# Performance work log

Hardware: AMD Instinct MI355X
Metric: run time of the kernel (lower is better)

## Reference

```python
import jax, jax.numpy as jnp
import numpy as np

A0 = 0.5291772105638411
KE = 14.399645351950548
KEHALF = KE / 2.0


def _softplus_inverse(x):
    return float(np.log(np.expm1(x)))


def setup_inputs() -> dict:
    key = jax.random.key(0)
    k_nb, k_mask, k_z, k_r = jax.random.split(key, 4)
    B, A, K = 16, 1024, 1023
    neighbors = jax.random.randint(k_nb, (B, A, K), 0, A)
    neighbor_mask = (jax.random.uniform(k_mask, (B, A, K)) > 0.1).astype(jnp.float32)
    atomic_numbers = jax.random.randint(k_z, (B, A), 1, 95)
    r_ij = jax.random.uniform(k_r, (B, A, K), minval=0.5, maxval=10.0, dtype=jnp.float32)
    p = jnp.float32
    params = {
        "_adiv": jnp.full((1,), _softplus_inverse(1.0 / (0.8854 * A0)), p),
        "_apow": jnp.full((1,), _softplus_inverse(0.23), p),
        "_c1": jnp.full((1,), _softplus_inverse(0.1818), p),
        "_c2": jnp.full((1,), _softplus_inverse(0.5099), p),
        "_c3": jnp.full((1,), _softplus_inverse(0.2802), p),
        "_c4": jnp.full((1,), _softplus_inverse(0.02817), p),
        "_a1": jnp.full((1,), _softplus_inverse(3.2), p),
        "_a2": jnp.full((1,), _softplus_inverse(0.9423), p),
        "_a3": jnp.full((1,), _softplus_inverse(0.4028), p),
        "_a4": jnp.full((1,), _softplus_inverse(0.2016), p),
    }
    return dict(neighbors=neighbors, neighbor_mask=neighbor_mask,
                atomic_numbers=atomic_numbers, r_ij=r_ij, **params)


def reference(neighbors, neighbor_mask, atomic_numbers, r_ij,
              _adiv, _apow, _c1, _c2, _c3, _c4, _a1, _a2, _a3, _a4):
    sp = jax.nn.softplus
    B = neighbors.shape[0]
    Zf = atomic_numbers.astype(jnp.float32)            # [B, A]
    Zp = Zf ** sp(_apow)                               # [B, A] (param [1] broadcasts)
    bidx = jnp.arange(B)[:, None, None]                # batch index for gather
    # gather of symmetric pair quantities without materializing [B, A, A]:
    # a[b,i,j] = Zp[b,i] + Zp[b,j];  zizj[b,i,j] = Zf[b,i] * Zf[b,j]
    Zp_j = Zp[bidx, neighbors]                         # [B, A, K]
    Zf_j = Zf[bidx, neighbors]                         # [B, A, K]
    a = (Zp[:, :, None] + Zp_j) * sp(_adiv) * neighbor_mask
    zizj = Zf[:, :, None] * Zf_j * neighbor_mask
    # normalized mixture coefficients
    c1, c2, c3, c4 = sp(_c1), sp(_c2), sp(_c3), sp(_c4)
    csum = c1 + c2 + c3 + c4
    c1, c2, c3, c4 = c1 / csum, c2 / csum, c3 / csum, c4 / csum
    ar = a * r_ij
    f = (c1 * jnp.exp(-sp(_a1) * ar) + c2 * jnp.exp(-sp(_a2) * ar)
         + c3 * jnp.exp(-sp(_a3) * ar) + c4 * jnp.exp(-sp(_a4) * ar))
    valid = neighbor_mask != 0
    r_safe = jnp.where(valid, r_ij, 1.0)
    corr_ij = jnp.where(valid, KEHALF * f * zizj / r_safe, 0.0)
    return jnp.sum(corr_ij, axis=-1, keepdims=True)    # [B, A, 1]
```

## Files before the change

### kernel.cpp

```cpp
#include <hip/hip_runtime.h>
#include <math.h>

#define KEHALF_F 7.199822675975274f
#define A_ATOMS 1024
#define LOG2E_F 1.4426950408889634f
#define LN2_F   0.6931471805599453f

#if !__has_builtin(__builtin_amdgcn_exp2f)
extern "C" __device__ float __ocml_native_exp2_f32(float);
#endif
#if !__has_builtin(__builtin_amdgcn_logf)
extern "C" __device__ float __ocml_native_log2_f32(float);
#endif

__device__ __forceinline__ float fast_exp2(float x) {
#if __has_builtin(__builtin_amdgcn_exp2f)
    return __builtin_amdgcn_exp2f(x);
#else
    return __ocml_native_exp2_f32(x);
#endif
}
__device__ __forceinline__ float fast_log2(float x) {
#if __has_builtin(__builtin_amdgcn_logf)
    return __builtin_amdgcn_logf(x);
#else
    return __ocml_native_log2_f32(x);
#endif
}
__device__ __forceinline__ float softplus_f(float x) {
    return LN2_F * fast_log2(1.0f + fast_exp2(x * LOG2E_F));
}

__global__ __launch_bounds__(256) void zbl_pre_kernel(
    const int* __restrict__ atomic_numbers,
    const float* __restrict__ p_adiv, const float* __restrict__ p_apow,
    float2* __restrict__ tab, int n)
{
    const int i = blockIdx.x * 256 + threadIdx.x;
    if (i < n) {
        const float sp_apow = softplus_f(p_apow[0]);
        const float sp_adiv = softplus_f(p_adiv[0]);
        float zf = (float)atomic_numbers[i];
        tab[i] = make_float2(zf, fast_exp2(sp_apow * fast_log2(zf)) * sp_adiv);
    }
}

__global__ __launch_bounds__(512, 8) void zbl_main_kernel(
    const int* __restrict__ neighbors,
    const float* __restrict__ neighbor_mask,
    const float* __restrict__ r_ij,
    const float2* __restrict__ tab,
    const float* __restrict__ p_c1, const float* __restrict__ p_c2,
    const float* __restrict__ p_c3, const float* __restrict__ p_c4,
    const float* __restrict__ p_a1, const float* __restrict__ p_a2,
    const float* __restrict__ p_a3, const float* __restrict__ p_a4,
    float* __restrict__ out, int K)
{
    __shared__ float2 zz[A_ATOMS];

    const int tid = threadIdx.x;
    const int block_row_base = blockIdx.x << 4;
    const int b = block_row_base >> 10;

    ((float4*)zz)[tid] = ((const float4*)(tab + ((size_t)b << 10)))[tid];
    __syncthreads();

    float c1 = softplus_f(p_c1[0]), c2 = softplus_f(p_c2[0]);
    float c3 = softplus_f(p_c3[0]), c4 = softplus_f(p_c4[0]);
    const float inv_cs = 1.0f / (c1 + c2 + c3 + c4);
    c1 *= inv_cs; c2 *= inv_cs; c3 *= inv_cs; c4 *= inv_cs;
    const float b1 = -softplus_f(p_a1[0]) * LOG2E_F;
    const float b2 = -softplus_f(p_a2[0]) * LOG2E_F;
    const float b3 = -softplus_f(p_a3[0]) * LOG2E_F;
    const float b4 = -softplus_f(p_a4[0]) * LOG2E_F;

    const int wid  = tid >> 6;
    const int lane = tid & 63;

#define ZBL_TERM(J, M, R)                                                   \
    {                                                                       \
        float2 zj = zz[(J)];                                                \
        float ar = (ziy + zj.y) * (M) * (R);                                \
        float fe = c1 * fast_exp2(b1 * ar) + c2 * fast_exp2(b2 * ar)        \
                 + c3 * fast_exp2(b3 * ar) + c4 * fast_exp2(b4 * ar);       \
        acc += fe * __fdividef(zix * zj.x * (M), (R));                      \
    }

    #pragma unroll 1
    for (int p = 0; p < 2; ++p) {
        const int row = block_row_base + wid + (p << 3);

        const float2 zi = zz[row & (A_ATOMS - 1)];
        const float zix = KEHALF_F * zi.x;
        const float ziy = zi.y;

        const size_t base = (size_t)row * K;
        const int f = (int)((4 - (int)(base & 3)) & 3);
        const int ngroups = (K - f) >> 2;
        const int tailc   = (K - f) & 3;

        const int*   nb = neighbors     + base;
        const float* mk = neighbor_mask + base;
        const float* rr = r_ij          + base;
        const int4*   nb4 = (const int4*)  (nb + f);
        const float4* mk4 = (const float4*)(mk + f);
        const float4* rr4 = (const float4*)(rr + f);

        float acc = 0.0f;

        const int g0 = lane, g1 = lane + 64, g2 = lane + 128, g3 = lane + 192;
        const int g3c  = g3 < ngroups ? g3 : (ngroups - 1);
        const float w3 = g3 < ngroups ? 1.0f : 0.0f;

        int4   j0 = nb4[g0], j1 = nb4[g1], j2 = nb4[g2], j3 = nb4[g3c];
        float4 m0 = mk4[g0], m1 = mk4[g1], m2 = mk4[g2], m3 = mk4[g3c];
        float4 r0 = rr4[g0], r1 = rr4[g1], r2 = rr4[g2], r3 = rr4[g3c];
        m3.x *= w3; m3.y *= w3; m3.z *= w3; m3.w *= w3;

        ZBL_TERM(j0.x, m0.x, r0.x); ZBL_TERM(j0.y, m0.y, r0.y);
        ZBL_TERM(j0.z, m0.z, r0.z); ZBL_TERM(j0.w, m0.w, r0.w);
        ZBL_TERM(j1.x, m1.x, r1.x); ZBL_TERM(j1.y, m1.y, r1.y);
        ZBL_TERM(j1.z, m1.z, r1.z); ZBL_TERM(j1.w, m1.w, r1.w);
        ZBL_TERM(j2.x, m2.x, r2.x); ZBL_TERM(j2.y, m2.y, r2.y);
        ZBL_TERM(j2.z, m2.z, r2.z); ZBL_TERM(j2.w, m2.w, r2.w);
        ZBL_TERM(j3.x, m3.x, r3.x); ZBL_TERM(j3.y, m3.y, r3.y);
        ZBL_TERM(j3.z, m3.z, r3.z); ZBL_TERM(j3.w, m3.w, r3.w);

        int e = -1;
        if (lane < f)              e = lane;
        else if (lane - f < tailc) e = f + (ngroups << 2) + (lane - f);
        if (e >= 0) {
            int   j = nb[e];
            float m = mk[e];
            float r = rr[e];
            ZBL_TERM(j, m, r);
        }

        #pragma unroll
        for (int off = 32; off > 0; off >>= 1)
            acc += __shfl_down(acc, off, 64);
        if (lane == 0)
            out[row] = acc;
    }
#undef ZBL_TERM
}

extern "C" void kernel_launch(void* const* d_in, const int* in_sizes, int n_in,
                              void* d_out, int out_size, void* d_ws, size_t ws_size,
                              hipStream_t stream) {
    const int*   neighbors      = (const int*)  d_in[0];
    const float* neighbor_mask  = (const float*)d_in[1];
    const int*   atomic_numbers = (const int*)  d_in[2];
    const float* r_ij           = (const float*)d_in[3];

    float*  out = (float*)d_out;
    float2* tab = (float2*)d_ws;

    const int n = in_sizes[2];
    const int K = in_sizes[0] / n;

    zbl_pre_kernel<<<(n + 255) / 256, 256, 0, stream>>>(
        atomic_numbers, (const float*)d_in[4], (const float*)d_in[5], tab, n);

    zbl_main_kernel<<<n / 16, 512, 0, stream>>>(
        neighbors, neighbor_mask, r_ij, tab,
        (const float*)d_in[6], (const float*)d_in[7],
        (const float*)d_in[8], (const float*)d_in[9],
        (const float*)d_in[10], (const float*)d_in[11],
        (const float*)d_in[12], (const float*)d_in[13],
        out, K);
}
```

Baseline: 254.3 us.

## Software-pipeline row loads with double-buffered registers and 4 rows per wave

Each wave now handles four rows with 256-thread blocks, prefetching the next row's neighbor, mask and distance vectors into a second register set while the current row computes. The scalar tail is loaded unconditionally with a clamped index, the division becomes a hardware reciprocal, and four independent accumulators break the add dependency chain. The mask multiply is dropped from the exponent argument, and the table load is issued before the parameter softplus setup. The goal is to hide global-memory latency within a wave, at the cost of higher register pressure and fewer waves per block. Approximate reciprocal precision is also slightly lower.

```diff
diff --git a/kernel.cpp b/kernel.cpp
--- a/kernel.cpp
+++ b/kernel.cpp
@@ -25,6 +25,13 @@
     return __builtin_amdgcn_logf(x);
 #else
     return __ocml_native_log2_f32(x);
+#endif
+}
+__device__ __forceinline__ float fast_rcp(float x) {
+#if __has_builtin(__builtin_amdgcn_rcpf)
+    return __builtin_amdgcn_rcpf(x);
+#else
+    return __frcp_rn(x);
 #endif
 }
 __device__ __forceinline__ float softplus_f(float x) {
@@ -45,7 +52,95 @@
     }
 }
 
-__global__ __launch_bounds__(512, 8) void zbl_main_kernel(
+struct RowData {
+    int4   j0, j1, j2, j3;
+    float4 m0, m1, m2, m3;
+    float4 r0, r1, r2, r3;
+    float  w3;
+    int    js; float ms, rs;
+    int    row;
+};
+
+__device__ __forceinline__ void load_row(
+    RowData& d, int row,
+    const int* __restrict__ nbg, const float* __restrict__ mkg,
+    const float* __restrict__ rrg, int K, int lane)
+{
+    d.row = row;
+    const size_t base = (size_t)row * K;
+    const int f = (int)((4 - (int)(base & 3)) & 3);
+    const int ngroups = (K - f) >> 2;
+    const int tailc   = (K - f) & 3;
+
+    const int*   nb = nbg + base;
+    const float* mk = mkg + base;
+    const float* rr = rrg + base;
+    const int4*   nb4 = (const int4*)  (nb + f);
+    const float4* mk4 = (const float4*)(mk + f);
+    const float4* rr4 = (const float4*)(rr + f);
+
+    const int g0 = lane, g1 = lane + 64, g2 = lane + 128, g3 = lane + 192;
+    const int g3c = g3 < ngroups ? g3 : (ngroups - 1);
+    d.w3 = g3 < ngroups ? 1.0f : 0.0f;
+
+    d.j0 = nb4[g0]; d.j1 = nb4[g1]; d.j2 = nb4[g2]; d.j3 = nb4[g3c];
+    d.m0 = mk4[g0]; d.m1 = mk4[g1]; d.m2 = mk4[g2]; d.m3 = mk4[g3c];
+    d.r0 = rr4[g0]; d.r1 = rr4[g1]; d.r2 = rr4[g2]; d.r3 = rr4[g3c];
+
+    int e = -1;
+    if (lane < f)              e = lane;
+    else if (lane - f < tailc) e = f + (ngroups << 2) + (lane - f);
+    const int ec = e < 0 ? 0 : e;
+    d.js = nb[ec];
+    d.rs = rr[ec];
+    float msv = mk[ec];
+    d.ms = e >= 0 ? msv : 0.0f;
+}
+
+__device__ __forceinline__ void compute_row(
+    const RowData& d, const float2* zz,
+    float c1, float c2, float c3, float c4,
+    float b1, float b2, float b3, float b4,
+    float* __restrict__ out, int lane)
+{
+    const float2 zi = zz[d.row & (A_ATOMS - 1)];
+    const float zix = KEHALF_F * zi.x;
+    const float ziy = zi.y;
+
+    float acc0 = 0.0f, acc1 = 0.0f, acc2 = 0.0f, acc3 = 0.0f;
+
+#define ZBL_TERM(ACC, J, M, R)                                              \
+    {                                                                       \
+        float2 zj = zz[(J)];                                                \
+        float ar = (ziy + zj.y) * (R);            \
+        float fe = c1 * fast_exp2(b1 * ar) + c2 * fast_exp2(b2 * ar)        \
+                 + c3 * fast_exp2(b3 * ar) + c4 * fast_exp2(b4 * ar);       \
+        ACC += fe * (zix * zj.x * (M)) * fast_rcp(R);                       \
+    }
+
+    float4 m3 = d.m3;
+    m3.x *= d.w3; m3.y *= d.w3; m3.z *= d.w3; m3.w *= d.w3;
+
+    ZBL_TERM(acc0, d.j0.x, d.m0.x, d.r0.x); ZBL_TERM(acc1, d.j0.y, d.m0.y, d.r0.y);
+    ZBL_TERM(acc2, d.j0.z, d.m0.z, d.r0.z); ZBL_TERM(acc3, d.j0.w, d.m0.w, d.r0.w);
+    ZBL_TERM(acc0, d.j1.x, d.m1.x, d.r1.x); ZBL_TERM(acc1, d.j1.y, d.m1.y, d.r1.y);
+    ZBL_TERM(acc2, d.j1.z, d.m1.z, d.r1.z); ZBL_TERM(acc3, d.j1.w, d.m1.w, d.r1.w);
+    ZBL_TERM(acc0, d.j2.x, d.m2.x, d.r2.x); ZBL_TERM(acc1, d.j2.y, d.m2.y, d.r2.y);
+    ZBL_TERM(acc2, d.j2.z, d.m2.z, d.r2.z); ZBL_TERM(acc3, d.j2.w, d.m2.w, d.r2.w);
+    ZBL_TERM(acc0, d.j3.x, m3.x,   d.r3.x); ZBL_TERM(acc1, d.j3.y, m3.y,   d.r3.y);
+    ZBL_TERM(acc2, d.j3.z, m3.z,   d.r3.z); ZBL_TERM(acc3, d.j3.w, m3.w,   d.r3.w);
+    ZBL_TERM(acc0, d.js,   d.ms,   d.rs);
+#undef ZBL_TERM
+
+    float acc = (acc0 + acc1) + (acc2 + acc3);
+    #pragma unroll
+    for (int off = 32; off > 0; off >>= 1)
+        acc += __shfl_down(acc, off, 64);
+    if (lane == 0)
+        out[d.row] = acc;
+}
+
+__global__ __launch_bounds__(256) void zbl_main_kernel(
     const int* __restrict__ neighbors,
     const float* __restrict__ neighbor_mask,
     const float* __restrict__ r_ij,
@@ -62,8 +157,9 @@
     const int block_row_base = blockIdx.x << 4;
     const int b = block_row_base >> 10;
 
-    ((float4*)zz)[tid] = ((const float4*)(tab + ((size_t)b << 10)))[tid];
-    __syncthreads();
+    const float4* tabf4 = (const float4*)(tab + ((size_t)b << 10));
+    float4 t0 = tabf4[tid];
+    float4 t1 = tabf4[tid + 256];
 
     float c1 = softplus_f(p_c1[0]), c2 = softplus_f(p_c2[0]);
     float c3 = softplus_f(p_c3[0]), c4 = softplus_f(p_c4[0]);
@@ -74,75 +170,23 @@
     const float b3 = -softplus_f(p_a3[0]) * LOG2E_F;
     const float b4 = -softplus_f(p_a4[0]) * LOG2E_F;
 
+    ((float4*)zz)[tid]       = t0;
+    ((float4*)zz)[tid + 256] = t1;
+    __syncthreads();
+
     const int wid  = tid >> 6;
     const int lane = tid & 63;
-
-#define ZBL_TERM(J, M, R)                                                   \
-    {                                                                       \
-        float2 zj = zz[(J)];                                                \
-        float ar = (ziy + zj.y) * (M) * (R);                                \
-        float fe = c1 * fast_exp2(b1 * ar) + c2 * fast_exp2(b2 * ar)        \
-                 + c3 * fast_exp2(b3 * ar) + c4 * fast_exp2(b4 * ar);       \
-        acc += fe * __fdividef(zix * zj.x * (M), (R));                      \
-    }
-
-    #pragma unroll 1
-    for (int p = 0; p < 2; ++p) {
-        const int row = block_row_base + wid + (p << 3);
-
-        const float2 zi = zz[row & (A_ATOMS - 1)];
-        const float zix = KEHALF_F * zi.x;
-        const float ziy = zi.y;
-
-        const size_t base = (size_t)row * K;
-        const int f = (int)((4 - (int)(base & 3)) & 3);
-        const int ngroups = (K - f) >> 2;
-        const int tailc   = (K - f) & 3;
-
-        const int*   nb = neighbors     + base;
-        const float* mk = neighbor_mask + base;
-        const float* rr = r_ij          + base;
-        const int4*   nb4 = (const int4*)  (nb + f);
-        const float4* mk4 = (const float4*)(mk + f);
-        const float4* rr4 = (const float4*)(rr + f);
-
-        float acc = 0.0f;
-
-        const int g0 = lane, g1 = lane + 64, g2 = lane + 128, g3 = lane + 192;
-        const int g3c  = g3 < ngroups ? g3 : (ngroups - 1);
-        const float w3 = g3 < ngroups ? 1.0f : 0.0f;
-
-        int4   j0 = nb4[g0], j1 = nb4[g1], j2 = nb4[g2], j3 = nb4[g3c];
-        float4 m0 = mk4[g0], m1 = mk4[g1], m2 = mk4[g2], m3 = mk4[g3c];
-        float4 r0 = rr4[g0], r1 = rr4[g1], r2 = rr4[g2], r3 = rr4[g3c];
-        m3.x *= w3; m3.y *= w3; m3.z *= w3; m3.w *= w3;
-
-        ZBL_TERM(j0.x, m0.x, r0.x); ZBL_TERM(j0.y, m0.y, r0.y);
-        ZBL_TERM(j0.z, m0.z, r0.z); ZBL_TERM(j0.w, m0.w, r0.w);
-        ZBL_TERM(j1.x, m1.x, r1.x); ZBL_TERM(j1.y, m1.y, r1.y);
-        ZBL_TERM(j1.z, m1.z, r1.z); ZBL_TERM(j1.w, m1.w, r1.w);
-        ZBL_TERM(j2.x, m2.x, r2.x); ZBL_TERM(j2.y, m2.y, r2.y);
-        ZBL_TERM(j2.z, m2.z, r2.z); ZBL_TERM(j2.w, m2.w, r2.w);
-        ZBL_TERM(j3.x, m3.x, r3.x); ZBL_TERM(j3.y, m3.y, r3.y);
-        ZBL_TERM(j3.z, m3.z, r3.z); ZBL_TERM(j3.w, m3.w, r3.w);
-
-        int e = -1;
-        if (lane < f)              e = lane;
-        else if (lane - f < tailc) e = f + (ngroups << 2) + (lane - f);
-        if (e >= 0) {
-            int   j = nb[e];
-            float m = mk[e];
-            float r = rr[e];
-            ZBL_TERM(j, m, r);
-        }
-
-        #pragma unroll
-        for (int off = 32; off > 0; off >>= 1)
-            acc += __shfl_down(acc, off, 64);
-        if (lane == 0)
-            out[row] = acc;
-    }
-#undef ZBL_TERM
+    const int r0 = block_row_base + (wid << 2);
+
+    RowData A, B;
+    load_row(A, r0 + 0, neighbors, neighbor_mask, r_ij, K, lane);
+    load_row(B, r0 + 1, neighbors, neighbor_mask, r_ij, K, lane);
+    compute_row(A, zz, c1, c2, c3, c4, b1, b2, b3, b4, out, lane);
+    load_row(A, r0 + 2, neighbors, neighbor_mask, r_ij, K, lane);
+    compute_row(B, zz, c1, c2, c3, c4, b1, b2, b3, b4, out, lane);
+    load_row(B, r0 + 3, neighbors, neighbor_mask, r_ij, K, lane);
+    compute_row(A, zz, c1, c2, c3, c4, b1, b2, b3, b4, out, lane);
+    compute_row(B, zz, c1, c2, c3, c4, b1, b2, b3, b4, out, lane);
 }
 
 extern "C" void kernel_launch(void* const* d_in, const int* in_sizes, int n_in,
@@ -162,7 +206,7 @@
     zbl_pre_kernel<<<(n + 255) / 256, 256, 0, stream>>>(
         atomic_numbers, (const float*)d_in[4], (const float*)d_in[5], tab, n);
 
-    zbl_main_kernel<<<n / 16, 512, 0, stream>>>(
+    zbl_main_kernel<<<n / 16, 256, 0, stream>>>(
         neighbors, neighbor_mask, r_ij, tab,
         (const float*)d_in[6], (const float*)d_in[7],
         (const float*)d_in[8], (const float*)d_in[9],
```

Result: faster. 224.0 us (-11.9%).

## Drop LDS table staging, gather neighbor Z directly from global, one row per wave

Applied to the files above, without the earlier changes.

Removes the shared-memory staging of the per-batch Z table and the block barrier, and has each wave handle a single row in 256-thread blocks. Neighbor table entries are gathered straight from global memory (L1/L2-resident) after all stream loads are issued up front, including the scalar tail. It also uses the hardware reciprocal instead of division, drops the mask multiply inside the exponent argument, and splits the sum into four accumulators. The cost is more scattered global or cache gathers in place of LDS reads, in exchange for more memory-level parallelism and no barrier.

```diff
diff --git a/kernel.cpp b/kernel.cpp
--- a/kernel.cpp
+++ b/kernel.cpp
@@ -27,6 +27,13 @@
     return __ocml_native_log2_f32(x);
 #endif
 }
+__device__ __forceinline__ float fast_rcp(float x) {
+#if __has_builtin(__builtin_amdgcn_rcpf)
+    return __builtin_amdgcn_rcpf(x);
+#else
+    return __frcp_rn(x);
+#endif
+}
 __device__ __forceinline__ float softplus_f(float x) {
     return LN2_F * fast_log2(1.0f + fast_exp2(x * LOG2E_F));
 }
@@ -45,7 +52,7 @@
     }
 }
 
-__global__ __launch_bounds__(512, 8) void zbl_main_kernel(
+__global__ __launch_bounds__(256, 4) void zbl_main_kernel(
     const int* __restrict__ neighbors,
     const float* __restrict__ neighbor_mask,
     const float* __restrict__ r_ij,
@@ -56,14 +63,46 @@
     const float* __restrict__ p_a3, const float* __restrict__ p_a4,
     float* __restrict__ out, int K)
 {
-    __shared__ float2 zz[A_ATOMS];
+    const int tid  = threadIdx.x;
+    const int lane = tid & 63;
+    const int row  = (blockIdx.x << 2) + (tid >> 6);
+    const int b    = row >> 10;
+    const float2* __restrict__ tb = tab + ((size_t)b << 10);
 
-    const int tid = threadIdx.x;
-    const int block_row_base = blockIdx.x << 4;
-    const int b = block_row_base >> 10;
+    const size_t base = (size_t)row * K;
+    const int f = (int)((4 - (int)(base & 3)) & 3);
+    const int ngroups = (K - f) >> 2;
+    const int tailc   = (K - f) & 3;
 
-    ((float4*)zz)[tid] = ((const float4*)(tab + ((size_t)b << 10)))[tid];
-    __syncthreads();
+    const int*   nb = neighbors     + base;
+    const float* mk = neighbor_mask + base;
+    const float* rr = r_ij          + base;
+    const int4*   nb4 = (const int4*)  (nb + f);
+    const float4* mk4 = (const float4*)(mk + f);
+    const float4* rr4 = (const float4*)(rr + f);
+
+    const int g0 = lane, g1 = lane + 64, g2 = lane + 128, g3 = lane + 192;
+    const int g3c  = g3 < ngroups ? g3 : 0;
+    const float w3 = g3 < ngroups ? 1.0f : 0.0f;
+
+    int e = -1;
+    if (lane < f)              e = lane;
+    else if (lane - f < tailc) e = f + (ngroups << 2) + (lane - f);
+    const int ec = e < 0 ? 0 : e;
+
+    int4   j0 = nb4[g0], j1 = nb4[g1], j2 = nb4[g2], j3 = nb4[g3c];
+    float4 m0 = mk4[g0], m1 = mk4[g1], m2 = mk4[g2], m3 = mk4[g3c];
+    float4 r0 = rr4[g0], r1 = rr4[g1], r2 = rr4[g2], r3 = rr4[g3c];
+    int   js = nb[ec];
+    float ms = mk[ec];
+    float rs = rr[ec];
+
+    float2 zi  = tb[row & (A_ATOMS - 1)];
+    float2 z00 = tb[j0.x], z01 = tb[j0.y], z02 = tb[j0.z], z03 = tb[j0.w];
+    float2 z10 = tb[j1.x], z11 = tb[j1.y], z12 = tb[j1.z], z13 = tb[j1.w];
+    float2 z20 = tb[j2.x], z21 = tb[j2.y], z22 = tb[j2.z], z23 = tb[j2.w];
+    float2 z30 = tb[j3.x], z31 = tb[j3.y], z32 = tb[j3.z], z33 = tb[j3.w];
+    float2 zs  = tb[js];
 
     float c1 = softplus_f(p_c1[0]), c2 = softplus_f(p_c2[0]);
     float c3 = softplus_f(p_c3[0]), c4 = softplus_f(p_c4[0]);
@@ -74,75 +113,39 @@
     const float b3 = -softplus_f(p_a3[0]) * LOG2E_F;
     const float b4 = -softplus_f(p_a4[0]) * LOG2E_F;
 
-    const int wid  = tid >> 6;
-    const int lane = tid & 63;
+    const float zix = KEHALF_F * zi.x;
+    const float ziy = zi.y;
 
-#define ZBL_TERM(J, M, R)                                                   \
+    m3.x *= w3; m3.y *= w3; m3.z *= w3; m3.w *= w3;
+    if (e < 0) ms = 0.0f;
+
+    float acc0 = 0.0f, acc1 = 0.0f, acc2 = 0.0f, acc3 = 0.0f;
+
+#define ZBL_TERM(ACC, ZJ, M, R)                                             \
     {                                                                       \
-        float2 zj = zz[(J)];                                                \
-        float ar = (ziy + zj.y) * (M) * (R);                                \
+        float ar = (ziy + (ZJ).y) * (R);          \
         float fe = c1 * fast_exp2(b1 * ar) + c2 * fast_exp2(b2 * ar)        \
                  + c3 * fast_exp2(b3 * ar) + c4 * fast_exp2(b4 * ar);       \
-        acc += fe * __fdividef(zix * zj.x * (M), (R));                      \
+        ACC += fe * (zix * (ZJ).x * (M)) * fast_rcp(R);                     \
     }
 
-    #pragma unroll 1
-    for (int p = 0; p < 2; ++p) {
-        const int row = block_row_base + wid + (p << 3);
+    ZBL_TERM(acc0, z00, m0.x, r0.x); ZBL_TERM(acc1, z01, m0.y, r0.y);
+    ZBL_TERM(acc2, z02, m0.z, r0.z); ZBL_TERM(acc3, z03, m0.w, r0.w);
+    ZBL_TERM(acc0, z10, m1.x, r1.x); ZBL_TERM(acc1, z11, m1.y, r1.y);
+    ZBL_TERM(acc2, z12, m1.z, r1.z); ZBL_TERM(acc3, z13, m1.w, r1.w);
+    ZBL_TERM(acc0, z20, m2.x, r2.x); ZBL_TERM(acc1, z21, m2.y, r2.y);
+    ZBL_TERM(acc2, z22, m2.z, r2.z); ZBL_TERM(acc3, z23, m2.w, r2.w);
+    ZBL_TERM(acc0, z30, m3.x, r3.x); ZBL_TERM(acc1, z31, m3.y, r3.y);
+    ZBL_TERM(acc2, z32, m3.z, r3.z); ZBL_TERM(acc3, z33, m3.w, r3.w);
+    ZBL_TERM(acc0, zs,  ms,   rs);
+#undef ZBL_TERM
 
-        const float2 zi = zz[row & (A_ATOMS - 1)];
-        const float zix = KEHALF_F * zi.x;
-        const float ziy = zi.y;
-
-        const size_t base = (size_t)row * K;
-        const int f = (int)((4 - (int)(base & 3)) & 3);
-        const int ngroups = (K - f) >> 2;
-        const int tailc   = (K - f) & 3;
-
-        const int*   nb = neighbors     + base;
-        const float* mk = neighbor_mask + base;
-        const float* rr = r_ij          + base;
-        const int4*   nb4 = (const int4*)  (nb + f);
-        const float4* mk4 = (const float4*)(mk + f);
-        const float4* rr4 = (const float4*)(rr + f);
-
-        float acc = 0.0f;
-
-        const int g0 = lane, g1 = lane + 64, g2 = lane + 128, g3 = lane + 192;
-        const int g3c  = g3 < ngroups ? g3 : (ngroups - 1);
-        const float w3 = g3 < ngroups ? 1.0f : 0.0f;
-
-        int4   j0 = nb4[g0], j1 = nb4[g1], j2 = nb4[g2], j3 = nb4[g3c];
-        float4 m0 = mk4[g0], m1 = mk4[g1], m2 = mk4[g2], m3 = mk4[g3c];
-        float4 r0 = rr4[g0], r1 = rr4[g1], r2 = rr4[g2], r3 = rr4[g3c];
-        m3.x *= w3; m3.y *= w3; m3.z *= w3; m3.w *= w3;
-
-        ZBL_TERM(j0.x, m0.x, r0.x); ZBL_TERM(j0.y, m0.y, r0.y);
-        ZBL_TERM(j0.z, m0.z, r0.z); ZBL_TERM(j0.w, m0.w, r0.w);
-        ZBL_TERM(j1.x, m1.x, r1.x); ZBL_TERM(j1.y, m1.y, r1.y);
-        ZBL_TERM(j1.z, m1.z, r1.z); ZBL_TERM(j1.w, m1.w, r1.w);
-        ZBL_TERM(j2.x, m2.x, r2.x); ZBL_TERM(j2.y, m2.y, r2.y);
-        ZBL_TERM(j2.z, m2.z, r2.z); ZBL_TERM(j2.w, m2.w, r2.w);
-        ZBL_TERM(j3.x, m3.x, r3.x); ZBL_TERM(j3.y, m3.y, r3.y);
-        ZBL_TERM(j3.z, m3.z, r3.z); ZBL_TERM(j3.w, m3.w, r3.w);
-
-        int e = -1;
-        if (lane < f)              e = lane;
-        else if (lane - f < tailc) e = f + (ngroups << 2) + (lane - f);
-        if (e >= 0) {
-            int   j = nb[e];
-            float m = mk[e];
-            float r = rr[e];
-            ZBL_TERM(j, m, r);
-        }
-
-        #pragma unroll
-        for (int off = 32; off > 0; off >>= 1)
-            acc += __shfl_down(acc, off, 64);
-        if (lane == 0)
-            out[row] = acc;
-    }
-#undef ZBL_TERM
+    float acc = (acc0 + acc1) + (acc2 + acc3);
+    #pragma unroll
+    for (int off = 32; off > 0; off >>= 1)
+        acc += __shfl_down(acc, off, 64);
+    if (lane == 0)
+        out[row] = acc;
 }
 
 extern "C" void kernel_launch(void* const* d_in, const int* in_sizes, int n_in,
@@ -162,7 +165,7 @@
     zbl_pre_kernel<<<(n + 255) / 256, 256, 0, stream>>>(
         atomic_numbers, (const float*)d_in[4], (const float*)d_in[5], tab, n);
 
-    zbl_main_kernel<<<n / 16, 512, 0, stream>>>(
+    zbl_main_kernel<<<n / 4, 256, 0, stream>>>(
         neighbors, neighbor_mask, r_ij, tab,
         (const float*)d_in[6], (const float*)d_in[7],
         (const float*)d_in[8], (const float*)d_in[9],
```

Result: faster. 217.9 us (-14.3%).

## Double-buffer row streaming into LDS via direct global-to-LDS loads

Applied to the files above, without the earlier changes.

Restructures the main kernel so each wave processes 16 rows and streams neighbor, mask and distance data for the next rows into a per-wave double-buffered LDS area using global_load_lds, with vmcnt waits to overlap loads with compute. Blocks shrink to 128 threads with a large LDS footprint, and the division is replaced by a hardware reciprocal. This aims to hide memory latency of the 200MB stream, but the large LDS use lowers occupancy, and the vmcnt(15) count is hand-tuned to the 15 loads issued per staged row.

```diff
diff --git a/kernel.cpp b/kernel.cpp
--- a/kernel.cpp
+++ b/kernel.cpp
@@ -5,6 +5,9 @@
 #define A_ATOMS 1024
 #define LOG2E_F 1.4426950408889634f
 #define LN2_F   0.6931471805599453f
+#define NISS    5
+#define ABYTES  (NISS * 1024)
+#define ROWS_PER_WAVE 16
 
 #if !__has_builtin(__builtin_amdgcn_exp2f)
 extern "C" __device__ float __ocml_native_exp2_f32(float);
@@ -27,8 +30,22 @@
     return __ocml_native_log2_f32(x);
 #endif
 }
+__device__ __forceinline__ float fast_rcp(float x) {
+#if __has_builtin(__builtin_amdgcn_rcpf)
+    return __builtin_amdgcn_rcpf(x);
+#else
+    return __frcp_rn(x);
+#endif
+}
 __device__ __forceinline__ float softplus_f(float x) {
     return LN2_F * fast_log2(1.0f + fast_exp2(x * LOG2E_F));
+}
+
+__device__ __forceinline__ void gload_lds16(const void* g, void* l) {
+    __builtin_amdgcn_global_load_lds(
+        (const __attribute__((address_space(1))) void*)g,
+        (__attribute__((address_space(3))) void*)l,
+        16, 0, 0);
 }
 
 __global__ __launch_bounds__(256) void zbl_pre_kernel(
@@ -45,7 +62,25 @@
     }
 }
 
-__global__ __launch_bounds__(512, 8) void zbl_main_kernel(
+__device__ __forceinline__ void stage_row(
+    int row, char* lb,
+    const int* __restrict__ nb, const float* __restrict__ mk,
+    const float* __restrict__ rr, int K, int Ntot, int lane)
+{
+    const int base = row * K;
+    const int al   = base & ~3;
+    const int cap  = Ntot - 4;
+    #pragma unroll
+    for (int i = 0; i < NISS; ++i) {
+        int e = al + (i << 8) + (lane << 2);
+        if (e > cap) e = cap;
+        gload_lds16(nb + e, lb + 0 * ABYTES + (i << 10));
+        gload_lds16(mk + e, lb + 1 * ABYTES + (i << 10));
+        gload_lds16(rr + e, lb + 2 * ABYTES + (i << 10));
+    }
+}
+
+__global__ __launch_bounds__(128) void zbl_main_kernel(
     const int* __restrict__ neighbors,
     const float* __restrict__ neighbor_mask,
     const float* __restrict__ r_ij,
@@ -54,16 +89,15 @@
     const float* __restrict__ p_c3, const float* __restrict__ p_c4,
     const float* __restrict__ p_a1, const float* __restrict__ p_a2,
     const float* __restrict__ p_a3, const float* __restrict__ p_a4,
-    float* __restrict__ out, int K)
+    float* __restrict__ out, int K, int Ntot)
 {
     __shared__ float2 zz[A_ATOMS];
-
-    const int tid = threadIdx.x;
-    const int block_row_base = blockIdx.x << 4;
-    const int b = block_row_base >> 10;
-
-    ((float4*)zz)[tid] = ((const float4*)(tab + ((size_t)b << 10)))[tid];
-    __syncthreads();
+    __shared__ char   stg[2][2][3][ABYTES];
+    __shared__ float  res[2 * ROWS_PER_WAVE];
+
+    const int tid  = threadIdx.x;
+    const int wid  = tid >> 6;
+    const int lane = tid & 63;
 
     float c1 = softplus_f(p_c1[0]), c2 = softplus_f(p_c2[0]);
     float c3 = softplus_f(p_c3[0]), c4 = softplus_f(p_c4[0]);
@@ -74,75 +108,70 @@
     const float b3 = -softplus_f(p_a3[0]) * LOG2E_F;
     const float b4 = -softplus_f(p_a4[0]) * LOG2E_F;
 
-    const int wid  = tid >> 6;
-    const int lane = tid & 63;
-
-#define ZBL_TERM(J, M, R)                                                   \
-    {                                                                       \
-        float2 zj = zz[(J)];                                                \
-        float ar = (ziy + zj.y) * (M) * (R);                                \
-        float fe = c1 * fast_exp2(b1 * ar) + c2 * fast_exp2(b2 * ar)        \
-                 + c3 * fast_exp2(b3 * ar) + c4 * fast_exp2(b4 * ar);       \
-        acc += fe * __fdividef(zix * zj.x * (M), (R));                      \
-    }
-
-    #pragma unroll 1
-    for (int p = 0; p < 2; ++p) {
-        const int row = block_row_base + wid + (p << 3);
+    const int bidx = blockIdx.x >> 5;
+    {
+        const float4* ts = (const float4*)(tab + ((size_t)bidx << 10));
+        float4* zd = (float4*)zz;
+        #pragma unroll
+        for (int t = 0; t < 4; ++t) zd[tid + (t << 7)] = ts[tid + (t << 7)];
+    }
+    __syncthreads();
+
+    const int wrow0 = (blockIdx.x * 2 + wid) << 4;
+    char* my_stg0 = &stg[wid][0][0][0];
+    char* my_stg1 = &stg[wid][1][0][0];
+
+    stage_row(wrow0 + 0, my_stg0, neighbors, neighbor_mask, r_ij, K, Ntot, lane);
+    stage_row(wrow0 + 1, my_stg1, neighbors, neighbor_mask, r_ij, K, Ntot, lane);
+
+    for (int r = 0; r < ROWS_PER_WAVE; ++r) {
+        if (r < ROWS_PER_WAVE - 1) {
+            asm volatile("s_waitcnt vmcnt(15)" ::: "memory");
+        } else {
+            asm volatile("s_waitcnt vmcnt(0)" ::: "memory");
+        }
+        __builtin_amdgcn_sched_barrier(0);
+
+        const int row  = wrow0 + r;
+        const int off  = (row * K) & 3;
+        const int bsel = r & 1;
+        const int*   nbp = (const int*)  &stg[wid][bsel][0][0];
+        const float* mkp = (const float*)&stg[wid][bsel][1][0];
+        const float* rrp = (const float*)&stg[wid][bsel][2][0];
 
         const float2 zi = zz[row & (A_ATOMS - 1)];
         const float zix = KEHALF_F * zi.x;
         const float ziy = zi.y;
 
-        const size_t base = (size_t)row * K;
-        const int f = (int)((4 - (int)(base & 3)) & 3);
-        const int ngroups = (K - f) >> 2;
-        const int tailc   = (K - f) & 3;
-
-        const int*   nb = neighbors     + base;
-        const float* mk = neighbor_mask + base;
-        const float* rr = r_ij          + base;
-        const int4*   nb4 = (const int4*)  (nb + f);
-        const float4* mk4 = (const float4*)(mk + f);
-        const float4* rr4 = (const float4*)(rr + f);
-
-        float acc = 0.0f;
-
-        const int g0 = lane, g1 = lane + 64, g2 = lane + 128, g3 = lane + 192;
-        const int g3c  = g3 < ngroups ? g3 : (ngroups - 1);
-        const float w3 = g3 < ngroups ? 1.0f : 0.0f;
-
-        int4   j0 = nb4[g0], j1 = nb4[g1], j2 = nb4[g2], j3 = nb4[g3c];
-        float4 m0 = mk4[g0], m1 = mk4[g1], m2 = mk4[g2], m3 = mk4[g3c];
-        float4 r0 = rr4[g0], r1 = rr4[g1], r2 = rr4[g2], r3 = rr4[g3c];
-        m3.x *= w3; m3.y *= w3; m3.z *= w3; m3.w *= w3;
-
-        ZBL_TERM(j0.x, m0.x, r0.x); ZBL_TERM(j0.y, m0.y, r0.y);
-        ZBL_TERM(j0.z, m0.z, r0.z); ZBL_TERM(j0.w, m0.w, r0.w);
-        ZBL_TERM(j1.x, m1.x, r1.x); ZBL_TERM(j1.y, m1.y, r1.y);
-        ZBL_TERM(j1.z, m1.z, r1.z); ZBL_TERM(j1.w, m1.w, r1.w);
-        ZBL_TERM(j2.x, m2.x, r2.x); ZBL_TERM(j2.y, m2.y, r2.y);
-        ZBL_TERM(j2.z, m2.z, r2.z); ZBL_TERM(j2.w, m2.w, r2.w);
-        ZBL_TERM(j3.x, m3.x, r3.x); ZBL_TERM(j3.y, m3.y, r3.y);
-        ZBL_TERM(j3.z, m3.z, r3.z); ZBL_TERM(j3.w, m3.w, r3.w);
-
-        int e = -1;
-        if (lane < f)              e = lane;
-        else if (lane - f < tailc) e = f + (ngroups << 2) + (lane - f);
-        if (e >= 0) {
-            int   j = nb[e];
-            float m = mk[e];
-            float r = rr[e];
-            ZBL_TERM(j, m, r);
+        float accA = 0.0f, accB = 0.0f;
+        #pragma unroll
+        for (int i = 0; i < 16; ++i) {
+            const int e = lane + (i << 6);
+            const int s = off + e;
+            int   j  = nbp[s];
+            float m  = mkp[s];
+            float rv = rrp[s];
+            if (e >= K) m = 0.0f;
+            float2 zj = zz[j];
+            float ar = (ziy + zj.y) * rv;
+            float fe = c1 * fast_exp2(b1 * ar) + c2 * fast_exp2(b2 * ar)
+                     + c3 * fast_exp2(b3 * ar) + c4 * fast_exp2(b4 * ar);
+            float t = fe * (zix * zj.x * m) * fast_rcp(rv);
+            if (i & 1) accB += t; else accA += t;
         }
-
+        float acc = accA + accB;
         #pragma unroll
-        for (int off = 32; off > 0; off >>= 1)
-            acc += __shfl_down(acc, off, 64);
-        if (lane == 0)
-            out[row] = acc;
-    }
-#undef ZBL_TERM
+        for (int o = 32; o > 0; o >>= 1)
+            acc += __shfl_down(acc, o, 64);
+        if (lane == 0) res[(wid << 4) + r] = acc;
+
+        if (r + 2 < ROWS_PER_WAVE)
+            stage_row(wrow0 + r + 2, bsel ? my_stg1 : my_stg0,
+                      neighbors, neighbor_mask, r_ij, K, Ntot, lane);
+    }
+
+    if (lane < ROWS_PER_WAVE)
+        out[wrow0 + lane] = res[(wid << 4) + lane];
 }
 
 extern "C" void kernel_launch(void* const* d_in, const int* in_sizes, int n_in,
@@ -158,15 +187,17 @@
 
     const int n = in_sizes[2];
     const int K = in_sizes[0] / n;
+    const int Ntot = n * K;
 
     zbl_pre_kernel<<<(n + 255) / 256, 256, 0, stream>>>(
         atomic_numbers, (const float*)d_in[4], (const float*)d_in[5], tab, n);
 
-    zbl_main_kernel<<<n / 16, 512, 0, stream>>>(
+    const int nwaves = n / ROWS_PER_WAVE;
+    zbl_main_kernel<<<nwaves / 2, 128, 0, stream>>>(
         neighbors, neighbor_mask, r_ij, tab,
         (const float*)d_in[6], (const float*)d_in[7],
         (const float*)d_in[8], (const float*)d_in[9],
         (const float*)d_in[10], (const float*)d_in[11],
         (const float*)d_in[12], (const float*)d_in[13],
-        out, K);
-}
+        out, K, Ntot);
+}
```

Measured after the change: 229.3 us. -9.8%, faster.
